# Kernel tuning notes

Hardware: AMD Instinct MI355X
Metric: run time of the kernel (lower is better)

The kernel has to match this reference:

```python
import jax, jax.numpy as jnp
import numpy as np

B, TQ, TK, F, H = 8, 2048, 2048, 1024, 1024


def setup_inputs() -> dict:
    key = jax.random.key(0)
    ks = jax.random.split(key, 9)
    scale = 1.0 / np.sqrt(F)
    query = jax.random.normal(ks[0], (B, TQ, F), dtype=jnp.float32)
    encoder_states = jax.random.normal(ks[1], (B, TK, F), dtype=jnp.float32)
    # boolean attention mask; True = keep. Random Bernoulli(0.5).
    target_mask = jax.random.randint(ks[2], (B, TQ, TK), 0, 2) > 0
    # Linear params (torch nn.Linear: y = x @ W.T + b); store W as [F, H] for x @ W.
    Wq = jax.random.normal(ks[3], (F, H), dtype=jnp.float32) * scale
    bq = jax.random.normal(ks[4], (H,), dtype=jnp.float32) * scale
    Wk = jax.random.normal(ks[5], (F, H), dtype=jnp.float32) * scale
    bk = jax.random.normal(ks[6], (H,), dtype=jnp.float32) * scale
    Wv = jax.random.normal(ks[7], (F, H), dtype=jnp.float32) * scale
    bv = jax.random.normal(ks[8], (H,), dtype=jnp.float32) * scale
    return {"query": query, "encoder_states": encoder_states, "target_mask": target_mask,
            "Wq": Wq, "bq": bq, "Wk": Wk, "bk": bk, "Wv": Wv, "bv": bv}


def reference(query, encoder_states, target_mask, Wq, bq, Wk, bk, Wv, bv):
    # init(): K/V projections of encoder states
    K = jnp.einsum('btf,fh->bth', encoder_states, Wk) + bk   # [B,TK,H]
    V = jnp.einsum('btf,fh->bth', encoder_states, Wv) + bv   # [B,TK,H]
    # forward()
    Q = jnp.einsum('btf,fh->bth', query, Wq) + bq            # [B,TQ,H]
    scores = jnp.einsum('bqh,bkh->bqk', Q, K) / jnp.sqrt(jnp.asarray(H, Q.dtype))
    scores = jnp.where(target_mask, scores, -jnp.inf)
    attn = jax.nn.softmax(scores, axis=-1)                   # [B,TQ,TK]
    return jnp.einsum('bqk,bkh->bqh', attn, V)               # [B,TQ,H]
```

## Files before the change

### kernel.cpp

```cpp
#include <hip/hip_runtime.h>

#define NB 8
#define TQv 2048
#define TKv 2048
#define FD 1024
#define HD 1024

typedef __attribute__((ext_vector_type(8))) short short8;
typedef __attribute__((ext_vector_type(8))) _Float16 half8;
typedef __attribute__((ext_vector_type(4))) float f32x4;

__device__ __forceinline__ short f2bf(float f) {
    union { float f; unsigned u; } v; v.f = f;
    unsigned r = v.u + 0x7FFFu + ((v.u >> 16) & 1u);
    return (short)(r >> 16);
}

__device__ __forceinline__ half8 as_h8(short8 v) {
    union { short8 s; half8 h; } u; u.s = v; return u.h;
}

__device__ __forceinline__ void async16(const short* g, short* l) {
    __builtin_amdgcn_global_load_lds(
        (const __attribute__((address_space(1))) unsigned int*)g,
        (__attribute__((address_space(3))) unsigned int*)l, 16, 0, 0);
}

__device__ __forceinline__ unsigned lds_off(void* p) {
    return (unsigned)(unsigned long long)(__attribute__((address_space(3))) char*)p;
}

#define BAR  __builtin_amdgcn_s_barrier()
#define SP1  __builtin_amdgcn_s_setprio(1)
#define SP0  __builtin_amdgcn_s_setprio(0)
#define SCB  __builtin_amdgcn_sched_barrier(0)
#define VMCNT(N) asm volatile("s_waitcnt vmcnt(" #N ")" ::: "memory")
#define LGKC(N)  asm volatile("s_waitcnt lgkmcnt(" #N ")" ::: "memory")

#define DSR(dst, addr, OFS) \
    asm volatile("ds_read_b128 %0, %1 offset:" OFS : "=v"(dst) : "v"(addr))

#define RD_ALO(BF) { DSR(aQ0[0][0], adA0[BF], "0");    DSR(aQ0[0][1], adA1[BF], "0"); \
                     DSR(aQ0[1][0], adA0[BF], "2048"); DSR(aQ0[1][1], adA1[BF], "2048"); \
                     DSR(aQ0[2][0], adA0[BF], "4096"); DSR(aQ0[2][1], adA1[BF], "4096"); \
                     DSR(aQ0[3][0], adA0[BF], "6144"); DSR(aQ0[3][1], adA1[BF], "6144"); }
#define RD_AHI(BF) { DSR(aQ1[0][0], adA0[BF], "8192");  DSR(aQ1[0][1], adA1[BF], "8192"); \
                     DSR(aQ1[1][0], adA0[BF], "10240"); DSR(aQ1[1][1], adA1[BF], "10240"); \
                     DSR(aQ1[2][0], adA0[BF], "12288"); DSR(aQ1[2][1], adA1[BF], "12288"); \
                     DSR(aQ1[3][0], adA0[BF], "14336"); DSR(aQ1[3][1], adA1[BF], "14336"); }
#define RD_BLO(BF) { DSR(bQ0[0][0], adB0[BF], "0");    DSR(bQ0[0][1], adB1[BF], "0"); \
                     DSR(bQ0[1][0], adB0[BF], "2048"); DSR(bQ0[1][1], adB1[BF], "2048"); }
#define RD_BHI(BF) { DSR(bQ1[0][0], adB0[BF], "4096"); DSR(bQ1[0][1], adB1[BF], "4096"); \
                     DSR(bQ1[1][0], adB0[BF], "6144"); DSR(bQ1[1][1], adB1[BF], "6144"); }

#define QMFMA(AQ, BQ, MO, NO) { \
    _Pragma("unroll") for (int ks = 0; ks < 2; ++ks) \
    _Pragma("unroll") for (int f = 0; f < 4; ++f) \
    _Pragma("unroll") for (int n = 0; n < 2; ++n) { \
        if constexpr (F16) \
            acc[(MO)+f][(NO)+n] = __builtin_amdgcn_mfma_f32_16x16x32_f16( \
                as_h8(AQ[f][ks]), as_h8(BQ[n][ks]), acc[(MO)+f][(NO)+n], 0, 0, 0); \
        else \
            acc[(MO)+f][(NO)+n] = __builtin_amdgcn_mfma_f32_16x16x32_bf16( \
                AQ[f][ks], BQ[n][ks], acc[(MO)+f][(NO)+n], 0, 0, 0); } }

#define STG_A(BF, H, REL) { \
    async16(gaBase + sH[2*(H)+0] + tofs + (REL), lbase + (BF)*32768 + (H)*8192); \
    async16(gaBase + sH[2*(H)+1] + tofs + (REL), lbase + (BF)*32768 + (H)*8192 + 4096); }
#define STG_B(BF, H, REL) { \
    async16(gbBase + sH[2*(H)+0] + tofs + (REL), lbase + (BF)*32768 + 16384 + (H)*8192); \
    async16(gbBase + sH[2*(H)+1] + tofs + (REL), lbase + (BF)*32768 + 16384 + (H)*8192 + 4096); }

template <bool F16>
__device__ __forceinline__ void gemm256_core(const short* __restrict__ A,
                                             const short* __restrict__ B,
                                             int ld, int K, char* smem,
                                             f32x4 acc[8][4], int tid) {
    const int wid = tid >> 6, lane = tid & 63;
    const int wm = wid >> 2, wn = wid & 3;
    const int l15 = lane & 15;

    const int kc8 = ((lane & 7) ^ (lane >> 3)) * 8;
    const short* gaBase = A + (size_t)(wid * 8 + (lane >> 3)) * ld + kc8;
    const short* gbBase = B + (size_t)(wid * 8 + (lane >> 3)) * ld + kc8;
    size_t sH[4];
#pragma unroll
    for (int k = 0; k < 4; ++k) sH[k] = (size_t)k * 64 * ld;
    short* lbase = (short*)smem + wid * 512;

    const int o0 = (((lane >> 4)    ) ^ (lane & 7)) * 16;
    const int o1 = (((lane >> 4) + 4) ^ (lane & 7)) * 16;
    unsigned aB_ = lds_off(smem) + wm * 16384 + l15 * 128;
    unsigned bB_ = lds_off(smem) + 32768 + (wn >> 1) * 16384 + (wn & 1) * 8192 + l15 * 128;
    unsigned adA0[2] = { aB_ + o0, aB_ + o0 + 65536u };
    unsigned adA1[2] = { aB_ + o1, aB_ + o1 + 65536u };
    unsigned adB0[2] = { bB_ + o0, bB_ + o0 + 65536u };
    unsigned adB1[2] = { bB_ + o1, bB_ + o1 + 65536u };

    int tofs = 0;
    STG_A(0, 0, 0); STG_A(0, 1, 0); STG_B(0, 0, 0); STG_B(0, 1, 0);
    STG_A(1, 0, 64); STG_A(1, 1, 64);
    SCB; VMCNT(4); BAR; SCB;

    short8 aQ0[4][2], aQ1[4][2], bQ0[2][2], bQ1[2][2];
    const int niter = K >> 7;
    for (int it = 0; it < niter; ++it) {
        const bool nl = (it != niter - 1);
        RD_ALO(0); RD_BLO(0);
        STG_B(1, 0, 64);
        SCB; LGKC(8); BAR; LGKC(0); SCB;
        SP1; QMFMA(aQ0, bQ0, 0, 0); SP0; SCB; BAR; SCB;
        RD_AHI(0);
        STG_B(1, 1, 64);
        SCB; BAR; LGKC(0); SCB;
        SP1; QMFMA(aQ1, bQ0, 4, 0); SP0; SCB; BAR; SCB;
        RD_BHI(0);
        if (nl) { STG_A(0, 0, 128); STG_A(0, 1, 128); }
        SCB; BAR; LGKC(0); SCB;
        SP1; QMFMA(aQ0, bQ1, 0, 2); QMFMA(aQ1, bQ1, 4, 2); SP0; SCB;
        if (nl) { VMCNT(4); } else { VMCNT(0); }
        BAR; SCB;
        RD_ALO(1); RD_BLO(1);
        if (nl) STG_B(0, 0, 128);
        SCB; LGKC(8); BAR; LGKC(0); SCB;
        SP1; QMFMA(aQ0, bQ0, 0, 0); SP0; SCB; BAR; SCB;
        RD_AHI(1);
        if (nl) STG_B(0, 1, 128);
        SCB; BAR; LGKC(0); SCB;
        SP1; QMFMA(aQ1, bQ0, 4, 0); SP0; SCB; BAR; SCB;
        RD_BHI(1);
        if (nl) { STG_A(1, 0, 192); STG_A(1, 1, 192); }
        SCB; BAR; LGKC(0); SCB;
        SP1; QMFMA(aQ0, bQ1, 0, 2); QMFMA(aQ1, bQ1, 4, 2); SP0; SCB;
        if (nl) VMCNT(4);
        BAR; SCB;
        tofs += 128;
    }
}


#define MB_BLKS   2048
#define CONV_BLKS 16384
#define CONV_END  (MB_BLKS + CONV_BLKS)
__global__ __launch_bounds__(256) void prep_kernel(const float* __restrict__ q,
                                                   const float* __restrict__ e,
                                                   const float* __restrict__ Wq,
                                                   const float* __restrict__ Wk,
                                                   const float* __restrict__ Wv,
                                                   const int* __restrict__ mask,
                                                   short* __restrict__ xq,
                                                   short* __restrict__ xe,
                                                   short* __restrict__ Wt,
                                                   unsigned long long* __restrict__ Mbits,
                                                   float* __restrict__ L) {
    __shared__ float tile[32][33];
    int bid = blockIdx.x, tid = threadIdx.x;
    if (bid < MB_BLKS) {
        int lane = tid & 63;
        if (bid < 64) L[bid * 256 + tid] = 0.f;
        int g = bid * 4 + (tid >> 6);
        const int* mp = mask + (size_t)g * 64 * 64;
        unsigned long long* op = Mbits + (size_t)g * 64;
#pragma unroll
        for (int i = 0; i < 16; ++i) {
            int v0 = mp[(i * 4 + 0) * 64 + lane];
            int v1 = mp[(i * 4 + 1) * 64 + lane];
            int v2 = mp[(i * 4 + 2) * 64 + lane];
            int v3 = mp[(i * 4 + 3) * 64 + lane];
            unsigned long long b0 = __ballot(v0 != 0);
            unsigned long long b1 = __ballot(v1 != 0);
            unsigned long long b2 = __ballot(v2 != 0);
            unsigned long long b3 = __ballot(v3 != 0);
            if (lane == 0) {
                op[i * 4 + 0] = b0; op[i * 4 + 1] = b1;
                op[i * 4 + 2] = b2; op[i * 4 + 3] = b3;
            }
        }
    } else if (bid < CONV_END) {
        int cb = bid - MB_BLKS;
        size_t i = (size_t)(cb & 8191) * 256 + tid;
        const float* src = (cb >> 13) ? e : q;
        short* dst = (cb >> 13) ? xe : xq;
        float4 a = ((const float4*)src)[2 * i];
        float4 b = ((const float4*)src)[2 * i + 1];
        short8 v;
        v[0] = f2bf(a.x); v[1] = f2bf(a.y); v[2] = f2bf(a.z); v[3] = f2bf(a.w);
        v[4] = f2bf(b.x); v[5] = f2bf(b.y); v[6] = f2bf(b.z); v[7] = f2bf(b.w);
        ((short8*)dst)[i] = v;
    } else {
        int t = bid - CONV_END;
        int z = t >> 10, r2 = t & 1023;
        const float* W = (z == 0) ? Wq : (z == 1) ? Wk : Wv;
        short* dst = Wt + (size_t)z * HD * FD;
        int h0 = (r2 & 31) * 32, f0 = (r2 >> 5) * 32;
        int tx = tid & 31, ty = tid >> 5;
        for (int j = ty; j < 32; j += 8)
            tile[j][tx] = W[(size_t)(f0 + j) * HD + h0 + tx];
        __syncthreads();
        for (int j = ty; j < 32; j += 8)
            dst[(size_t)(h0 + j) * FD + f0 + tx] = f2bf(tile[tx][j]);
    }
}

__global__ __launch_bounds__(512, 2) void projqk_kernel(const short* __restrict__ Xq,
                                                        const short* __restrict__ Xe,
                                                        const short* __restrict__ Wt3,
                                                        const float* __restrict__ bq,
                                                        const float* __restrict__ bk,
                                                        short* __restrict__ Q,
                                                        short* __restrict__ K) {
    extern __shared__ char smem[];
    int tid = threadIdx.x;
    int p = blockIdx.z;
    const short* X = p ? Xe : Xq;
    const short* Wt = Wt3 + (size_t)p * HD * FD;
    const float* bias = p ? bk : bq;
    short* O = p ? K : Q;
    int bid = blockIdx.x;
    int xcd = bid & 7, idx = bid >> 3;
    int n_t = idx & 3, m_t = (idx >> 2) * 8 + xcd;
    int tile_m = m_t * 256, tile_n = n_t * 256;
    f32x4 acc[8][4] = {};
    gemm256_core<false>(X + (size_t)tile_m * FD, Wt + (size_t)tile_n * FD, FD, FD, smem, acc, tid);
    int wid = tid >> 6, lane = tid & 63;
    int wm = wid >> 2, wn = wid & 3;
    int row0 = tile_m + wm * 128 + ((lane >> 4) << 2);
    int col0 = tile_n + wn * 64 + (lane & 15);
    float bv4[4];
#pragma unroll
    for (int n = 0; n < 4; ++n) bv4[n] = bias[col0 + n * 16];
#pragma unroll
    for (int m = 0; m < 8; ++m)
#pragma unroll
        for (int r = 0; r < 4; ++r) {
            size_t rowb = (size_t)(row0 + m * 16 + r) * HD;
#pragma unroll
            for (int n = 0; n < 4; ++n)
                O[rowb + col0 + n * 16] = f2bf(acc[m][n][r] + bv4[n]);
        }
}

__global__ __launch_bounds__(512, 2) void projv_kernel(const short* __restrict__ Xe,
                                                       const short* __restrict__ Wtv,
                                                       const float* __restrict__ bv,
                                                       short* __restrict__ Vt) {
    extern __shared__ char smem[];
    int tid = threadIdx.x;
    int bid = blockIdx.x;
    int b = bid & 7, i = bid >> 3;
    int m_t = i & 3, n_t = i >> 2;
    int tile_m = m_t * 256, tile_n = n_t * 256;
    const short* Xb = Xe + (size_t)b * TKv * FD;
    f32x4 acc[8][4] = {};
    gemm256_core<false>(Wtv + (size_t)tile_m * FD, Xb + (size_t)tile_n * FD, FD, FD, smem, acc, tid);
    short* Ob = Vt + (size_t)b * HD * TKv;
    int wid = tid >> 6, lane = tid & 63;
    int wm = wid >> 2, wn = wid & 3;
    int row0 = tile_m + wm * 128 + ((lane >> 4) << 2);
    int col0 = tile_n + wn * 64 + (lane & 15);
#pragma unroll
    for (int m = 0; m < 8; ++m)
#pragma unroll
        for (int r = 0; r < 4; ++r) {
            int gm = row0 + m * 16 + r;
            float bv_ = bv[gm];
#pragma unroll
            for (int n = 0; n < 4; ++n) {
                union { _Float16 h; short s; } cv;
                cv.h = (_Float16)(acc[m][n][r] + bv_);
                Ob[(size_t)gm * TKv + col0 + n * 16] = cv.s;
            }
        }
}

__global__ __launch_bounds__(512, 2) void score_kernel(const short* __restrict__ Q,
                                                       const short* __restrict__ K,
                                                       const unsigned long long* __restrict__ Mbits,
                                                       short* __restrict__ S,
                                                       float* __restrict__ L) {
    extern __shared__ char smem[];
    int tid = threadIdx.x;
    int bid = blockIdx.x;
    int b = bid & 7, i = bid >> 3;
    int n_t = i & 7, m_t = i >> 3;
    int tile_m = m_t * 256, tile_n = n_t * 256;
    const short* Aq = Q + (size_t)b * TQv * HD;
    const short* Bk = K + (size_t)b * TKv * HD;
    f32x4 acc[8][4] = {};
    gemm256_core<false>(Aq + (size_t)tile_m * HD, Bk + (size_t)tile_n * HD, HD, HD, smem, acc, tid);
    short* Sb = S + (size_t)b * TQv * TKv;
    float* Lb = L + (size_t)b * TQv;
    int wid = tid >> 6, lane = tid & 63;
    int wm = wid >> 2, wn = wid & 3;
    int l15 = lane & 15;
    int row0 = tile_m + wm * 128 + ((lane >> 4) << 2);
    int col0 = tile_n + wn * 64 + l15;

    {
        const unsigned long long* MbT = Mbits + (size_t)b * TQv * (TKv / 64)
                                        + (size_t)tile_m * (TKv / 64) + (tile_n >> 6);
        async16((const short*)(MbT + (size_t)(tid >> 1) * (TKv / 64) + (size_t)(tid & 1) * 2),
                (short*)smem + wid * 512);
    }
    __syncthreads();

#pragma unroll
    for (int m = 0; m < 8; ++m)
#pragma unroll
        for (int r = 0; r < 4; ++r) {
            int rl = wm * 128 + m * 16 + ((lane >> 4) << 2) + r;
            int gm = tile_m + rl;
            unsigned long long bits = *(const unsigned long long*)(smem + rl * 32 + wn * 8);
            float rs = 0.f;
#pragma unroll
            for (int n = 0; n < 4; ++n) {
                float pv = ((bits >> (n * 16 + l15)) & 1ULL)
                               ? exp2f(acc[m][n][r] * 0.04508422f - 5.77078016f) : 0.f;
                rs += pv;
                union { _Float16 h; short sh; } cv;
                cv.h = (_Float16)pv;
                Sb[(size_t)gm * TKv + col0 + n * 16] = cv.sh;
            }
            for (int sh = 1; sh < 16; sh <<= 1) rs += __shfl_xor(rs, sh);
            if (l15 == 0) atomicAdd(&Lb[gm], rs);
        }
}

__global__ __launch_bounds__(512, 2) void pv_kernel(const short* __restrict__ P,
                                                    const short* __restrict__ Vt,
                                                    const float* __restrict__ L,
                                                    float* __restrict__ Out) {
    extern __shared__ char smem[];
    int tid = threadIdx.x;
    int bid = blockIdx.x;
    int b = bid & 7, i = bid >> 3;
    int n_t = i & 3, m_t = i >> 2;
    int tile_m = m_t * 256, tile_n = n_t * 256;
    const short* Ap = P + (size_t)b * TQv * TKv;
    const short* Bv = Vt + (size_t)b * HD * TKv;
    const float* Lb = L + (size_t)b * TQv;
    f32x4 acc[8][4] = {};
    gemm256_core<true>(Ap + (size_t)tile_m * TKv, Bv + (size_t)tile_n * TKv, TKv, TKv, smem, acc, tid);
    float* Ob = Out + (size_t)b * TQv * HD;
    int wid = tid >> 6, lane = tid & 63;
    int wm = wid >> 2, wn = wid & 3;
    int row0 = tile_m + wm * 128 + ((lane >> 4) << 2);
    int col0 = tile_n + wn * 64 + (lane & 15);

    if (tid < 64)
        async16((const short*)(Lb + tile_m + tid * 4), (short*)smem);
    __syncthreads();

#pragma unroll
    for (int m = 0; m < 8; ++m)
#pragma unroll
        for (int r = 0; r < 4; ++r) {
            int rl = wm * 128 + m * 16 + ((lane >> 4) << 2) + r;
            int gm = tile_m + rl;
            float l = *(const float*)(smem + rl * 4);
            float inv = (l > 0.f) ? 1.f / l : 0.f;
#pragma unroll
            for (int n = 0; n < 4; ++n)
                Ob[(size_t)gm * HD + col0 + n * 16] = acc[m][n][r] * inv;
        }
}

extern "C" void kernel_launch(void* const* d_in, const int* in_sizes, int n_in,
                              void* d_out, int out_size, void* d_ws, size_t ws_size,
                              hipStream_t stream) {
    const float* query = (const float*)d_in[0];
    const float* enc   = (const float*)d_in[1];
    const int*   mask  = (const int*)d_in[2];
    const float* Wq    = (const float*)d_in[3];
    const float* bq    = (const float*)d_in[4];
    const float* Wk    = (const float*)d_in[5];
    const float* bk    = (const float*)d_in[6];
    const float* Wv    = (const float*)d_in[7];
    const float* bv    = (const float*)d_in[8];
    float* out = (float*)d_out;

    char* ws = (char*)d_ws;
    unsigned long long* Mbits = (unsigned long long*)(ws);
    float* L   = (float*)(ws + 4194304);
    short* Wt  = (short*)(ws + 4259840);
    short* Xq  = (short*)(ws + 10551296);
    short* Xe  = (short*)(ws + 44105728);
    short* S   = (short*)(ws + 10551296);
    short* Qb  = (short*)(ws + 77660160);
    short* Kb  = (short*)(ws + 111214592);
    short* Vt  = (short*)(ws + 144769024);
    (void)in_sizes; (void)n_in; (void)out_size; (void)ws_size;

    static bool inited = false;
    if (!inited) {
        hipFuncSetAttribute((const void*)projqk_kernel, hipFuncAttributeMaxDynamicSharedMemorySize, 131072);
        hipFuncSetAttribute((const void*)projv_kernel,  hipFuncAttributeMaxDynamicSharedMemorySize, 131072);
        hipFuncSetAttribute((const void*)score_kernel,  hipFuncAttributeMaxDynamicSharedMemorySize, 131072);
        hipFuncSetAttribute((const void*)pv_kernel,     hipFuncAttributeMaxDynamicSharedMemorySize, 131072);
        inited = true;
    }

    prep_kernel<<<dim3(MB_BLKS + CONV_BLKS + 3072), 256, 0, stream>>>(
        query, enc, Wq, Wk, Wv, mask, Xq, Xe, Wt, Mbits, L);
    projqk_kernel<<<dim3(256, 1, 2), 512, 131072, stream>>>(Xq, Xe, Wt, bq, bk, Qb, Kb);
    projv_kernel<<<dim3(256), 512, 131072, stream>>>(Xe, Wt + (size_t)2 * HD * FD, bv, Vt);
    score_kernel<<<dim3(512), 512, 131072, stream>>>(Qb, Kb, Mbits, S, L);
    pv_kernel<<<dim3(256), 512, 131072, stream>>>(S, Vt, L, out);
}
```

Baseline: 541.4 us.

## Software-pipeline GEMM LDS reads, vectorize mask packing and halve conversion blocks

The GEMM main loop is reordered so LDS fragment reads for the next sub-step are issued before the current MFMA group, with the first A/B-low read hoisted out of the loop. This is meant to overlap LDS latency with matrix math. The mask bit-packing now uses int4 loads and shuffle-OR reduction instead of four scalar loads and ballots. The fp32-to-bf16 conversion processes sixteen elements per thread with half as many blocks. The reordering adds register pressure and relies on correct wait counts for the LDS reads.

Measured after the change: 552.9 us. +2.1%, slower.

```diff
diff --git a/kernel.cpp b/kernel.cpp
--- a/kernel.cpp
+++ b/kernel.cpp
@@ -103,44 +103,46 @@
     SCB; VMCNT(4); BAR; SCB;
 
     short8 aQ0[4][2], aQ1[4][2], bQ0[2][2], bQ1[2][2];
+    RD_ALO(0); RD_BLO(0);
     const int niter = K >> 7;
     for (int it = 0; it < niter; ++it) {
         const bool nl = (it != niter - 1);
-        RD_ALO(0); RD_BLO(0);
         STG_B(1, 0, 64);
-        SCB; LGKC(8); BAR; LGKC(0); SCB;
+        SCB; BAR; LGKC(0); SCB;
+        RD_AHI(0);
         SP1; QMFMA(aQ0, bQ0, 0, 0); SP0; SCB; BAR; SCB;
-        RD_AHI(0);
         STG_B(1, 1, 64);
         SCB; BAR; LGKC(0); SCB;
-        SP1; QMFMA(aQ1, bQ0, 4, 0); SP0; SCB; BAR; SCB;
         RD_BHI(0);
-        if (nl) { STG_A(0, 0, 128); STG_A(0, 1, 128); }
-        SCB; BAR; LGKC(0); SCB;
-        SP1; QMFMA(aQ0, bQ1, 0, 2); QMFMA(aQ1, bQ1, 4, 2); SP0; SCB;
-        if (nl) { VMCNT(4); } else { VMCNT(0); }
+        SP1; QMFMA(aQ1, bQ0, 4, 0); SP0;
+        LGKC(0); SCB;
+        SP1; QMFMA(aQ0, bQ1, 0, 2); SP0; SCB; BAR; SCB;
+        if (nl) { STG_A(0, 0, 128); STG_A(0, 1, 128); SCB; VMCNT(4); }
+        else    { SCB; VMCNT(0); }
         BAR; SCB;
         RD_ALO(1); RD_BLO(1);
+        SP1; QMFMA(aQ1, bQ1, 4, 2); SP0; SCB; BAR; SCB;
         if (nl) STG_B(0, 0, 128);
-        SCB; LGKC(8); BAR; LGKC(0); SCB;
+        SCB; BAR; LGKC(0); SCB;
+        RD_AHI(1);
         SP1; QMFMA(aQ0, bQ0, 0, 0); SP0; SCB; BAR; SCB;
-        RD_AHI(1);
         if (nl) STG_B(0, 1, 128);
         SCB; BAR; LGKC(0); SCB;
-        SP1; QMFMA(aQ1, bQ0, 4, 0); SP0; SCB; BAR; SCB;
         RD_BHI(1);
-        if (nl) { STG_A(1, 0, 192); STG_A(1, 1, 192); }
-        SCB; BAR; LGKC(0); SCB;
-        SP1; QMFMA(aQ0, bQ1, 0, 2); QMFMA(aQ1, bQ1, 4, 2); SP0; SCB;
-        if (nl) VMCNT(4);
+        SP1; QMFMA(aQ1, bQ0, 4, 0); SP0;
+        LGKC(0); SCB;
+        SP1; QMFMA(aQ0, bQ1, 0, 2); SP0; SCB; BAR; SCB;
+        if (nl) { STG_A(1, 0, 192); STG_A(1, 1, 192); SCB; VMCNT(4); }
         BAR; SCB;
+        if (nl) { RD_ALO(0); RD_BLO(0); }
+        SP1; QMFMA(aQ1, bQ1, 4, 2); SP0; SCB; BAR; SCB;
         tofs += 128;
     }
 }
 
 
 #define MB_BLKS   2048
-#define CONV_BLKS 16384
+#define CONV_BLKS 8192
 #define CONV_END  (MB_BLKS + CONV_BLKS)
 __global__ __launch_bounds__(256) void prep_kernel(const float* __restrict__ q,
                                                    const float* __restrict__ e,
@@ -159,34 +161,34 @@
         int lane = tid & 63;
         if (bid < 64) L[bid * 256 + tid] = 0.f;
         int g = bid * 4 + (tid >> 6);
-        const int* mp = mask + (size_t)g * 64 * 64;
+        const int4* mp = (const int4*)(mask + (size_t)g * 64 * 64);
         unsigned long long* op = Mbits + (size_t)g * 64;
-#pragma unroll
+#pragma unroll 4
         for (int i = 0; i < 16; ++i) {
-            int v0 = mp[(i * 4 + 0) * 64 + lane];
-            int v1 = mp[(i * 4 + 1) * 64 + lane];
-            int v2 = mp[(i * 4 + 2) * 64 + lane];
-            int v3 = mp[(i * 4 + 3) * 64 + lane];
-            unsigned long long b0 = __ballot(v0 != 0);
-            unsigned long long b1 = __ballot(v1 != 0);
-            unsigned long long b2 = __ballot(v2 != 0);
-            unsigned long long b3 = __ballot(v3 != 0);
-            if (lane == 0) {
-                op[i * 4 + 0] = b0; op[i * 4 + 1] = b1;
-                op[i * 4 + 2] = b2; op[i * 4 + 3] = b3;
-            }
+            int4 v = mp[i * 64 + lane];
+            unsigned nib = (v.x != 0 ? 1u : 0u) | (v.y != 0 ? 2u : 0u)
+                         | (v.z != 0 ? 4u : 0u) | (v.w != 0 ? 8u : 0u);
+            unsigned long long val = (unsigned long long)nib << (4 * (lane & 15));
+            val |= __shfl_xor(val, 1);
+            val |= __shfl_xor(val, 2);
+            val |= __shfl_xor(val, 4);
+            val |= __shfl_xor(val, 8);
+            if ((lane & 15) == 0) op[i * 4 + (lane >> 4)] = val;
         }
     } else if (bid < CONV_END) {
         int cb = bid - MB_BLKS;
-        size_t i = (size_t)(cb & 8191) * 256 + tid;
-        const float* src = (cb >> 13) ? e : q;
-        short* dst = (cb >> 13) ? xe : xq;
-        float4 a = ((const float4*)src)[2 * i];
-        float4 b = ((const float4*)src)[2 * i + 1];
-        short8 v;
-        v[0] = f2bf(a.x); v[1] = f2bf(a.y); v[2] = f2bf(a.z); v[3] = f2bf(a.w);
-        v[4] = f2bf(b.x); v[5] = f2bf(b.y); v[6] = f2bf(b.z); v[7] = f2bf(b.w);
-        ((short8*)dst)[i] = v;
+        size_t i = (size_t)(cb & 4095) * 256 + tid;
+        const float* src = (cb >> 12) ? e : q;
+        short* dst = (cb >> 12) ? xe : xq;
+        const float4* s4 = (const float4*)src + i * 4;
+        float4 a = s4[0], b = s4[1], c = s4[2], d = s4[3];
+        short8 v0, v1;
+        v0[0] = f2bf(a.x); v0[1] = f2bf(a.y); v0[2] = f2bf(a.z); v0[3] = f2bf(a.w);
+        v0[4] = f2bf(b.x); v0[5] = f2bf(b.y); v0[6] = f2bf(b.z); v0[7] = f2bf(b.w);
+        v1[0] = f2bf(c.x); v1[1] = f2bf(c.y); v1[2] = f2bf(c.z); v1[3] = f2bf(c.w);
+        v1[4] = f2bf(d.x); v1[5] = f2bf(d.y); v1[6] = f2bf(d.z); v1[7] = f2bf(d.w);
+        ((short8*)dst)[i * 2]     = v0;
+        ((short8*)dst)[i * 2 + 1] = v1;
     } else {
         int t = bid - CONV_END;
         int z = t >> 10, r2 = t & 1023;
```
